# Kernel tuning notes

Hardware: AMD Instinct MI355X
Metric: run time of the kernel (lower is better)

Reference implementation:

```python
import jax, jax.numpy as jnp
import numpy as np

D_MODEL = 1024
NUM_HEADS = 16
D_HEAD = D_MODEL // NUM_HEADS
NEG_INF = float(np.finfo(np.float32).min)


def setup_inputs() -> dict:
    key = jax.random.key(0)
    ks = jax.random.split(key, 6)
    B, S = 2, 2048
    q = jax.random.normal(ks[0], (B, S, D_MODEL), dtype=jnp.float32)
    k = jax.random.normal(ks[1], (B, S, D_MODEL), dtype=jnp.float32)
    v = jax.random.normal(ks[2], (B, S, D_MODEL), dtype=jnp.float32)
    # causal boolean mask: True = attend
    attn_mask = jnp.tril(jnp.ones((S, S), dtype=bool))
    # nn.Linear(d_model, d_model, bias=False) weights: [out, in]; y = x @ W.T
    init_scale = 1.0 / np.sqrt(D_MODEL)
    Wq = jax.random.uniform(ks[3], (D_MODEL, D_MODEL), jnp.float32, -init_scale, init_scale)
    Wk = jax.random.uniform(ks[4], (D_MODEL, D_MODEL), jnp.float32, -init_scale, init_scale)
    Wv = jax.random.uniform(ks[5], (D_MODEL, D_MODEL), jnp.float32, -init_scale, init_scale)
    return {"query": q, "key": k, "value": v, "Wq": Wq, "Wk": Wk, "Wv": Wv,
            "attn_mask": attn_mask}


def _split_heads(x):
    # [B, S, D_MODEL] -> [B, H, S, d_head]
    B, S, _ = x.shape
    return x.reshape(B, S, NUM_HEADS, D_HEAD).transpose(0, 2, 1, 3)


def reference(query, key, value, Wq, Wk, Wv, attn_mask):
    B, Sq, _ = query.shape
    Sk = key.shape[1]
    q = _split_heads(query @ Wq.T)   # [B, H, Sq, dh]
    k = _split_heads(key @ Wk.T)     # [B, H, Sk, dh]
    v = _split_heads(value @ Wv.T)   # [B, H, Sk, dh]
    scale = 1.0 / np.sqrt(D_HEAD)
    scores = jnp.einsum('bhqd,bhkd->bhqk', q, k) * scale  # [B, H, Sq, Sk]
    scores = jnp.where(attn_mask[None, None, :, :], scores, NEG_INF)
    attn_weights = jax.nn.softmax(scores, axis=-1)
    ctx = jnp.einsum('bhqk,bhkd->bhqd', attn_weights, v)   # [B, H, Sq, dh]
    context = ctx.transpose(0, 2, 1, 3).reshape(B, Sq, D_MODEL)
    return context, attn_weights
```

## Files before the change

### kernel.cpp

```cpp
#include <hip/hip_runtime.h>
#include <hip/hip_bf16.h>

#define B_ 2
#define H_ 16
#define S_ 2048
#define DH_ 64
#define DM_ 1024
#define BH_ (B_*H_)
#define CTX_ELEMS (B_*S_*DM_)
#define ATTNW_ELEMS ((size_t)BH_*S_*S_)
#define HEAD_ELEMS (S_*DH_)

typedef __attribute__((ext_vector_type(4))) float  f32x4;
typedef __attribute__((ext_vector_type(8))) short  short8;
typedef __attribute__((ext_vector_type(4))) unsigned short ush4;
typedef unsigned short u16;
typedef unsigned int u32;

__device__ __forceinline__ u16 f2bf(float f) {
  union { __hip_bfloat16 h; u16 u; } cv;
  cv.h = __float2bfloat16(f);
  return cv.u;
}
__device__ __forceinline__ float bf2f(u16 u) {
  union { unsigned int i; float f; } cv;
  cv.i = ((unsigned int)u) << 16;
  return cv.f;
}

__device__ __forceinline__ void gload_lds16(const u16* g, u16* l) {
  __builtin_amdgcn_global_load_lds(
      (const __attribute__((address_space(1))) u32*)g,
      (__attribute__((address_space(3))) u32*)l, 16, 0, 0);
}

__global__ __launch_bounds__(256) void convert_all(
    const float* __restrict__ q, const float* __restrict__ k, const float* __restrict__ v,
    const float* __restrict__ wq, const float* __restrict__ wk, const float* __restrict__ wv,
    u16* __restrict__ xb, u16* __restrict__ wb)
{
  const int t = blockIdx.y;
  const float* s; u16* d; int nblk;
  if (t < 3) {
    s = (t == 0) ? wq : (t == 1) ? wk : wv;
    d = wb + (size_t)t * (DM_ * DM_);
    nblk = 512;
  } else {
    s = (t == 3) ? q : (t == 4) ? k : v;
    d = xb + (size_t)(t - 3) * ((size_t)B_ * S_ * DM_);
    nblk = 2048;
  }
  if (blockIdx.x >= nblk) return;
  const int i = (blockIdx.x * 256 + threadIdx.x) * 8;
  f32x4 a = *(const f32x4*)(s + i);
  f32x4 b = *(const f32x4*)(s + i + 4);
  short8 p;
#pragma unroll
  for (int j = 0; j < 4; ++j) { p[j] = (short)f2bf(a[j]); p[4 + j] = (short)f2bf(b[j]); }
  *(short8*)(d + i) = p;
}

__global__ __launch_bounds__(256) void proj_gemm(
    const u16* __restrict__ Xb, const u16* __restrict__ Wb,
    u16* __restrict__ O0, u16* __restrict__ O1, u16* __restrict__ O2)
{
  u16* O = (blockIdx.z == 0) ? O0 : (blockIdx.z == 1) ? O1 : O2;
  const u16* A = Xb + (size_t)blockIdx.z * ((size_t)B_ * S_ * DM_);
  const u16* W = Wb + (size_t)blockIdx.z * (DM_ * DM_);

  const int m0 = blockIdx.x * 128;
  const int n0 = blockIdx.y * 128;

  __shared__ u16 As[128 * 32];
  __shared__ u16 Bs[128 * 32];

  const int tid  = threadIdx.x;
  const int lane = tid & 63;
  const int w    = tid >> 6;
  const int wr   = w >> 1, wc = w & 1;
  const int l15  = lane & 15, l4 = lane >> 4;

  f32x4 acc[4][4];
#pragma unroll
  for (int i = 0; i < 4; ++i)
#pragma unroll
    for (int j = 0; j < 4; ++j) acc[i][j] = (f32x4){0.f, 0.f, 0.f, 0.f};

  const int srow = lane >> 2;
  const int scol = (lane & 3) * 8;
  const int ca = w * 2;
  const u16* ga0 = A + (size_t)(m0 + ca * 16 + srow) * DM_ + scol;
  const u16* ga1 = A + (size_t)(m0 + ca * 16 + 16 + srow) * DM_ + scol;
  const u16* gb0 = W + (size_t)(n0 + ca * 16 + srow) * DM_ + scol;
  const u16* gb1 = W + (size_t)(n0 + ca * 16 + 16 + srow) * DM_ + scol;

  for (int kb = 0; kb < DM_ / 32; ++kb) {
    const int k0 = kb * 32;
    gload_lds16(ga0 + k0, &As[ca * 512]);
    gload_lds16(ga1 + k0, &As[ca * 512 + 512]);
    gload_lds16(gb0 + k0, &Bs[ca * 512]);
    gload_lds16(gb1 + k0, &Bs[ca * 512 + 512]);
    __syncthreads();
    short8 af[4], bfr[4];
#pragma unroll
    for (int i = 0; i < 4; ++i)
      af[i] = *(const short8*)&As[(wr * 64 + i * 16 + l15) * 32 + l4 * 8];
#pragma unroll
    for (int j = 0; j < 4; ++j)
      bfr[j] = *(const short8*)&Bs[(wc * 64 + j * 16 + l15) * 32 + l4 * 8];
#pragma unroll
    for (int i = 0; i < 4; ++i)
#pragma unroll
      for (int j = 0; j < 4; ++j)
        acc[i][j] = __builtin_amdgcn_mfma_f32_16x16x32_bf16(af[i], bfr[j], acc[i][j], 0, 0, 0);
    __syncthreads();
  }

#pragma unroll
  for (int i = 0; i < 4; ++i) {
#pragma unroll
    for (int j = 0; j < 4; ++j) {
#pragma unroll
      for (int r = 0; r < 4; ++r) {
        const int grow = m0 + wr * 64 + i * 16 + l4 * 4 + r;
        const int gcol = n0 + wc * 64 + j * 16 + l15;
        const int b = grow >> 11, s = grow & (S_ - 1);
        const int h = gcol >> 6,  d = gcol & (DH_ - 1);
        O[(size_t)((b << 4) + h) * HEAD_ELEMS + (size_t)s * DH_ + d] = f2bf(acc[i][j][r]);
      }
    }
  }
}

__global__ __launch_bounds__(256) void transpose_v(const u16* __restrict__ vb,
                                                   u16* __restrict__ vt)
{
  __shared__ u16 T[64][72];
  const int bh = blockIdx.y;
  const int s0 = blockIdx.x * 64;
  const int tid = threadIdx.x;
  {
    const int sl = tid >> 2, dof = (tid & 3) * 16;
    const u16* src = vb + (size_t)bh * HEAD_ELEMS + (size_t)(s0 + sl) * DH_ + dof;
    *(short8*)&T[sl][dof]     = *(const short8*)(src);
    *(short8*)&T[sl][dof + 8] = *(const short8*)(src + 8);
  }
  __syncthreads();
  {
    const int dd = tid >> 2, sof = (tid & 3) * 16;
    u16* dst = vt + (size_t)bh * HEAD_ELEMS + (size_t)dd * S_ + s0 + sof;
    short8 t0, t1;
#pragma unroll
    for (int j = 0; j < 8; ++j) t0[j] = (short)T[sof + j][dd];
#pragma unroll
    for (int j = 0; j < 8; ++j) t1[j] = (short)T[sof + 8 + j][dd];
    *(short8*)(dst)     = t0;
    *(short8*)(dst + 8) = t1;
  }
}

#define PROW 2048
#define ATT_SMEM (16 * PROW * 2 + 16 * 4 + 64 * 4)

__global__ __launch_bounds__(256) void attn_kernel(
    const u16* __restrict__ qb, const u16* __restrict__ kb, const u16* __restrict__ vt,
    float* __restrict__ ctx, float* __restrict__ attnw)
{
  extern __shared__ u16 smem[];
  u16* P = smem;
  float* rinv    = (float*)(smem + 16 * PROW);
  float* partial = rinv + 16;

  const int lin = blockIdx.y * 128 + blockIdx.x;
  const int nl  = (lin & 7) * 512 + (lin >> 3);
  const int bh  = nl >> 7;
  const int qtl = nl & 127;
  const int qt  = 127 - qtl;

  const int tid = threadIdx.x;
  const int lane = tid & 63;
  const int w = tid >> 6;
  const int l15 = lane & 15, l4 = lane >> 4;

  const int NCC = ((qt * 16 + 16) + 127) >> 7;
  const int ncols = NCC << 7;
  const int qtmax = qt * 16 + 15;

  const u16* Qb = qb + (size_t)bh * HEAD_ELEMS + (size_t)(qt * 16) * DH_;
  const u16* Kb = kb + (size_t)bh * HEAD_ELEMS;
  const u16* Vt = vt + (size_t)bh * HEAD_ELEMS;

  const int qm = qtl;
  const int mcols = (((qm * 16 + 16) + 127) >> 7) << 7;
  float* zbase = attnw + (size_t)bh * ((size_t)S_ * S_) + (size_t)(qm * 16 + w * 4) * S_;
  const int zro = lane >> 5;
  const int zcl = (lane & 31) * 4;
  const f32x4 zv = (f32x4){0.f, 0.f, 0.f, 0.f};

  {
    short8 aQ0 = *(const short8*)(Qb + (size_t)l15 * DH_ + l4 * 8);
    short8 aQ1 = *(const short8*)(Qb + (size_t)l15 * DH_ + l4 * 8 + 32);
    const int qrow = l4 * 4;
    const int qabs = qt * 16 + qrow;
    float psum[4] = {0.f, 0.f, 0.f, 0.f};
    for (int ci = 0; ci < NCC; ++ci) {
      const int zc = mcols + (ci << 7);
      if (zc < S_) {
        __builtin_nontemporal_store(zv, (f32x4*)(zbase + (size_t)zro * S_ + zc + zcl));
        __builtin_nontemporal_store(zv, (f32x4*)(zbase + (size_t)(2 + zro) * S_ + zc + zcl));
      }
      const int col0 = (ci << 7) + w * 32;
#pragma unroll
      for (int t = 0; t < 2; ++t) {
        const int ct = col0 + t * 16;
        const int cg = ct + l15;
        if (ct <= qtmax) {
          const u16* kp = Kb + (size_t)cg * DH_ + l4 * 8;
          short8 b0 = *(const short8*)(kp);
          short8 b1 = *(const short8*)(kp + 32);
          f32x4 a0 = (f32x4){0.f, 0.f, 0.f, 0.f};
          f32x4 a1 = (f32x4){0.f, 0.f, 0.f, 0.f};
          a0 = __builtin_amdgcn_mfma_f32_16x16x32_bf16(aQ0, b0, a0, 0, 0, 0);
          a1 = __builtin_amdgcn_mfma_f32_16x16x32_bf16(aQ1, b1, a1, 0, 0, 0);
          const f32x4 a = a0 + a1;
#pragma unroll
          for (int r = 0; r < 4; ++r) {
            const float e = (cg <= qabs + r) ? __expf(a[r] * 0.125f) : 0.f;
            psum[r] += e;
            const int row = qrow + r;
            P[(row << 11) + (cg ^ ((row & 7) << 3))] = f2bf(e);
          }
        } else {
#pragma unroll
          for (int r = 0; r < 4; ++r) {
            const int row = qrow + r;
            P[(row << 11) + (cg ^ ((row & 7) << 3))] = 0;
          }
        }
      }
    }
#pragma unroll
    for (int r = 0; r < 4; ++r) {
      float s = psum[r];
      s += __shfl_xor(s, 1);
      s += __shfl_xor(s, 2);
      s += __shfl_xor(s, 4);
      s += __shfl_xor(s, 8);
      if (l15 == 0) partial[w * 16 + qrow + r] = s;
    }
  }
  __syncthreads();
  if (tid < 16) {
    const float l = partial[tid] + partial[16 + tid] + partial[32 + tid] + partial[48 + tid];
    rinv[tid] = 1.0f / l;
  }
  __syncthreads();

  if (w < 2) {
    for (int rr = 0; rr < 8; ++rr) {
      const int row = w * 8 + rr;
      const float inv = rinv[row];
      const int swz = (row & 7) << 3;
      const u16* prow = P + (row << 11);
      float* orow = attnw + (size_t)bh * ((size_t)S_ * S_) + (size_t)(qt * 16 + row) * S_;
      for (int c = 0; c < ncols; c += 256) {
        const int col = c + lane * 4;
        ush4 pv = *(const ush4*)(prow + (col ^ swz));
        const bool live = col < ncols;
        f32x4 o;
        o[0] = live ? bf2f(pv[0]) * inv : 0.f;
        o[1] = live ? bf2f(pv[1]) * inv : 0.f;
        o[2] = live ? bf2f(pv[2]) * inv : 0.f;
        o[3] = live ? bf2f(pv[3]) * inv : 0.f;
        if (live) __builtin_nontemporal_store(o, (f32x4*)(orow + col));
      }
    }
  } else {
    const int dq0 = (w - 2) * 2;
    f32x4 a00 = (f32x4){0.f, 0.f, 0.f, 0.f};
    f32x4 a01 = (f32x4){0.f, 0.f, 0.f, 0.f};
    f32x4 a10 = (f32x4){0.f, 0.f, 0.f, 0.f};
    f32x4 a11 = (f32x4){0.f, 0.f, 0.f, 0.f};
    const u16* vp0 = Vt + (size_t)(dq0 * 16 + l15) * S_ + l4 * 8;
    const u16* vp1 = vp0 + (size_t)16 * S_;
    const u16* prow = P + (l15 << 11);
    const int swz = (l15 & 7) << 3;
    for (int c = 0; c < ncols; c += 64) {
      short8 ap0 = *(const short8*)(prow + ((c + l4 * 8) ^ swz));
      short8 ap1 = *(const short8*)(prow + ((c + 32 + l4 * 8) ^ swz));
      short8 b00 = *(const short8*)(vp0 + c);
      short8 b01 = *(const short8*)(vp0 + c + 32);
      short8 b10 = *(const short8*)(vp1 + c);
      short8 b11 = *(const short8*)(vp1 + c + 32);
      a00 = __builtin_amdgcn_mfma_f32_16x16x32_bf16(ap0, b00, a00, 0, 0, 0);
      a10 = __builtin_amdgcn_mfma_f32_16x16x32_bf16(ap0, b10, a10, 0, 0, 0);
      a01 = __builtin_amdgcn_mfma_f32_16x16x32_bf16(ap1, b01, a01, 0, 0, 0);
      a11 = __builtin_amdgcn_mfma_f32_16x16x32_bf16(ap1, b11, a11, 0, 0, 0);
    }
    const f32x4 acc0 = a00 + a01;
    const f32x4 acc1 = a10 + a11;
    const int b = bh >> 4, h = bh & 15;
#pragma unroll
    for (int r = 0; r < 4; ++r) {
      const int rg = qt * 16 + l4 * 4 + r;
      const float inv = rinv[l4 * 4 + r];
      ctx[(size_t)(b * S_ + rg) * DM_ + h * 64 + dq0 * 16 + l15]        = acc0[r] * inv;
      ctx[(size_t)(b * S_ + rg) * DM_ + h * 64 + (dq0 + 1) * 16 + l15]  = acc1[r] * inv;
    }
  }
}

extern "C" void kernel_launch(void* const* d_in, const int* in_sizes, int n_in,
                              void* d_out, int out_size, void* d_ws, size_t ws_size,
                              hipStream_t stream) {
  const float* q  = (const float*)d_in[0];
  const float* k  = (const float*)d_in[1];
  const float* v  = (const float*)d_in[2];
  const float* Wq = (const float*)d_in[3];
  const float* Wk = (const float*)d_in[4];
  const float* Wv = (const float*)d_in[5];

  float* ctx   = (float*)d_out;
  float* attnw = ctx + CTX_ELEMS;

  u16* wb = (u16*)d_ws;
  u16* qb = wb + (size_t)3 * DM_ * DM_;
  u16* kb = qb + (size_t)BH_ * HEAD_ELEMS;
  u16* vb = kb + (size_t)BH_ * HEAD_ELEMS;
  u16* vt = vb + (size_t)BH_ * HEAD_ELEMS;
  u16* xb = (u16*)attnw;

  hipFuncSetAttribute(reinterpret_cast<const void*>(attn_kernel),
                      hipFuncAttributeMaxDynamicSharedMemorySize, ATT_SMEM);

  convert_all<<<dim3(2048, 6), 256, 0, stream>>>(q, k, v, Wq, Wk, Wv, xb, wb);
  proj_gemm<<<dim3(32, 8, 3), 256, 0, stream>>>(xb, wb, qb, kb, vb);
  transpose_v<<<dim3(32, 32), 256, 0, stream>>>(vb, vt);
  attn_kernel<<<dim3(128, 32), 256, ATT_SMEM, stream>>>(qb, kb, vt, ctx, attnw);
}
```

Before: 208.4 us.

## Make attention persistent with producer/consumer warps and double-buffered P tiles

Replaces the 4096 one-tile blocks with 256 persistent 512-thread blocks. Each block walks 16 query tiles of one head, strided so causal work is balanced. Four warps compute scores and exponentials into one of two LDS P buffers while the other four warps normalize and write attention weights, zero-fill the masked region, and do the PV MFMA for the previous tile. The goal is to overlap the QK/softmax phase with the store-heavy and PV phases and to cut launch and tail cost. The cost is 128 KB of LDS per block, so each CU holds far fewer blocks, and every tile step ends in a block-wide barrier.

```diff
diff --git a/kernel.cpp b/kernel.cpp
--- a/kernel.cpp
+++ b/kernel.cpp
@@ -159,153 +159,164 @@
   }
 }
 
-#define PROW 2048
-#define ATT_SMEM (16 * PROW * 2 + 16 * 4 + 64 * 4)
-
-__global__ __launch_bounds__(256) void attn_kernel(
+#define NTILES 16
+#define PBUF (16 * 2048)
+#define ATT_SMEM (2 * PBUF * 2 + 2 * 64 * 4)
+
+__global__ __launch_bounds__(512) void attn_kernel(
     const u16* __restrict__ qb, const u16* __restrict__ kb, const u16* __restrict__ vt,
     float* __restrict__ ctx, float* __restrict__ attnw)
 {
   extern __shared__ u16 smem[];
-  u16* P = smem;
-  float* rinv    = (float*)(smem + 16 * PROW);
-  float* partial = rinv + 16;
-
-  const int lin = blockIdx.y * 128 + blockIdx.x;
-  const int nl  = (lin & 7) * 512 + (lin >> 3);
-  const int bh  = nl >> 7;
-  const int qtl = nl & 127;
-  const int qt  = 127 - qtl;
+  u16* Pb = smem;
+  float* partial = (float*)(smem + 2 * PBUF);
+
+  const int lin = blockIdx.x;
+  const int nl  = (lin & 7) * 32 + (lin >> 3);
+  const int bh  = nl >> 3;
+  const int g   = nl & 7;
 
   const int tid = threadIdx.x;
   const int lane = tid & 63;
   const int w = tid >> 6;
   const int l15 = lane & 15, l4 = lane >> 4;
 
-  const int NCC = ((qt * 16 + 16) + 127) >> 7;
-  const int ncols = NCC << 7;
-  const int qtmax = qt * 16 + 15;
-
-  const u16* Qb = qb + (size_t)bh * HEAD_ELEMS + (size_t)(qt * 16) * DH_;
   const u16* Kb = kb + (size_t)bh * HEAD_ELEMS;
   const u16* Vt = vt + (size_t)bh * HEAD_ELEMS;
-
-  const int qm = qtl;
-  const int mcols = (((qm * 16 + 16) + 127) >> 7) << 7;
-  float* zbase = attnw + (size_t)bh * ((size_t)S_ * S_) + (size_t)(qm * 16 + w * 4) * S_;
-  const int zro = lane >> 5;
-  const int zcl = (lane & 31) * 4;
-  const f32x4 zv = (f32x4){0.f, 0.f, 0.f, 0.f};
-
-  {
-    short8 aQ0 = *(const short8*)(Qb + (size_t)l15 * DH_ + l4 * 8);
-    short8 aQ1 = *(const short8*)(Qb + (size_t)l15 * DH_ + l4 * 8 + 32);
-    const int qrow = l4 * 4;
-    const int qabs = qt * 16 + qrow;
-    float psum[4] = {0.f, 0.f, 0.f, 0.f};
-    for (int ci = 0; ci < NCC; ++ci) {
-      const int zc = mcols + (ci << 7);
-      if (zc < S_) {
-        __builtin_nontemporal_store(zv, (f32x4*)(zbase + (size_t)zro * S_ + zc + zcl));
-        __builtin_nontemporal_store(zv, (f32x4*)(zbase + (size_t)(2 + zro) * S_ + zc + zcl));
+  float* attnw_bh = attnw + (size_t)bh * ((size_t)S_ * S_);
+  const int bb = bh >> 4, hh = bh & 15;
+
+  for (int j = 0; j <= NTILES; ++j) {
+    __syncthreads();
+
+    if (w < 4) {
+      if (j < NTILES) {
+        const int qt = g + 8 * j;
+        const int NCC = j + 1;
+        const int qtmax = qt * 16 + 15;
+        const int buf = j & 1;
+        u16* P = Pb + buf * PBUF;
+        const u16* Qb = qb + (size_t)bh * HEAD_ELEMS + (size_t)(qt * 16) * DH_;
+
+        short8 aQ0 = *(const short8*)(Qb + (size_t)l15 * DH_ + l4 * 8);
+        short8 aQ1 = *(const short8*)(Qb + (size_t)l15 * DH_ + l4 * 8 + 32);
+        const int qrow = l4 * 4;
+        const int qabs = qt * 16 + qrow;
+        float psum[4] = {0.f, 0.f, 0.f, 0.f};
+        for (int ci = 0; ci < NCC; ++ci) {
+          const int col0 = (ci << 7) + w * 32;
+#pragma unroll
+          for (int t = 0; t < 2; ++t) {
+            const int ct = col0 + t * 16;
+            const int cg = ct + l15;
+            if (ct <= qtmax) {
+              const u16* kp = Kb + (size_t)cg * DH_ + l4 * 8;
+              short8 b0 = *(const short8*)(kp);
+              short8 b1 = *(const short8*)(kp + 32);
+              f32x4 a0 = (f32x4){0.f, 0.f, 0.f, 0.f};
+              f32x4 a1 = (f32x4){0.f, 0.f, 0.f, 0.f};
+              a0 = __builtin_amdgcn_mfma_f32_16x16x32_bf16(aQ0, b0, a0, 0, 0, 0);
+              a1 = __builtin_amdgcn_mfma_f32_16x16x32_bf16(aQ1, b1, a1, 0, 0, 0);
+              const f32x4 a = a0 + a1;
+#pragma unroll
+              for (int r = 0; r < 4; ++r) {
+                const float e = (cg <= qabs + r) ? __expf(a[r] * 0.125f) : 0.f;
+                psum[r] += e;
+                const int row = qrow + r;
+                P[(row << 11) + (cg ^ ((row & 7) << 3))] = f2bf(e);
+              }
+            } else {
+#pragma unroll
+              for (int r = 0; r < 4; ++r) {
+                const int row = qrow + r;
+                P[(row << 11) + (cg ^ ((row & 7) << 3))] = 0;
+              }
+            }
+          }
+        }
+#pragma unroll
+        for (int r = 0; r < 4; ++r) {
+          float s = psum[r];
+          s += __shfl_xor(s, 1);
+          s += __shfl_xor(s, 2);
+          s += __shfl_xor(s, 4);
+          s += __shfl_xor(s, 8);
+          if (l15 == 0) partial[buf * 64 + w * 16 + qrow + r] = s;
+        }
       }
-      const int col0 = (ci << 7) + w * 32;
-#pragma unroll
-      for (int t = 0; t < 2; ++t) {
-        const int ct = col0 + t * 16;
-        const int cg = ct + l15;
-        if (ct <= qtmax) {
-          const u16* kp = Kb + (size_t)cg * DH_ + l4 * 8;
-          short8 b0 = *(const short8*)(kp);
-          short8 b1 = *(const short8*)(kp + 32);
-          f32x4 a0 = (f32x4){0.f, 0.f, 0.f, 0.f};
-          f32x4 a1 = (f32x4){0.f, 0.f, 0.f, 0.f};
-          a0 = __builtin_amdgcn_mfma_f32_16x16x32_bf16(aQ0, b0, a0, 0, 0, 0);
-          a1 = __builtin_amdgcn_mfma_f32_16x16x32_bf16(aQ1, b1, a1, 0, 0, 0);
-          const f32x4 a = a0 + a1;
-#pragma unroll
-          for (int r = 0; r < 4; ++r) {
-            const float e = (cg <= qabs + r) ? __expf(a[r] * 0.125f) : 0.f;
-            psum[r] += e;
-            const int row = qrow + r;
-            P[(row << 11) + (cg ^ ((row & 7) << 3))] = f2bf(e);
+    } else if (j > 0) {
+      const int qt = g + 8 * (j - 1);
+      const int ncols = 128 * j;
+      const int buf = (j - 1) & 1;
+      const u16* P = Pb + buf * PBUF;
+      const float* pa = partial + buf * 64;
+
+      if (w < 6) {
+        const int cw = w - 4;
+        for (int rr = 0; rr < 8; ++rr) {
+          const int row = cw * 8 + rr;
+          const float inv = 1.0f / (pa[row] + pa[16 + row] + pa[32 + row] + pa[48 + row]);
+          const int swz = (row & 7) << 3;
+          const u16* prow = P + (row << 11);
+          float* orow = attnw_bh + (size_t)(qt * 16 + row) * S_;
+          for (int c = 0; c < ncols; c += 256) {
+            const int col = c + lane * 4;
+            ush4 pv = *(const ush4*)(prow + (col ^ swz));
+            const bool live = col < ncols;
+            f32x4 o;
+            o[0] = live ? bf2f(pv[0]) * inv : 0.f;
+            o[1] = live ? bf2f(pv[1]) * inv : 0.f;
+            o[2] = live ? bf2f(pv[2]) * inv : 0.f;
+            o[3] = live ? bf2f(pv[3]) * inv : 0.f;
+            if (live) __builtin_nontemporal_store(o, (f32x4*)(orow + col));
           }
-        } else {
-#pragma unroll
-          for (int r = 0; r < 4; ++r) {
-            const int row = qrow + r;
-            P[(row << 11) + (cg ^ ((row & 7) << 3))] = 0;
-          }
+        }
+        const int qm = 127 - qt;
+        const int mcols = S_ - ncols + 128;
+        const f32x4 zv = (f32x4){0.f, 0.f, 0.f, 0.f};
+        for (int rr = 0; rr < 8; ++rr) {
+          float* zrow = attnw_bh + (size_t)(qm * 16 + cw * 8 + rr) * S_;
+          for (int c = mcols + lane * 4; c < S_; c += 256)
+            __builtin_nontemporal_store(zv, (f32x4*)(zrow + c));
+        }
+      } else {
+        const int dq0 = (w - 6) * 2;
+        float invr[4];
+#pragma unroll
+        for (int r = 0; r < 4; ++r) {
+          const int row = l4 * 4 + r;
+          invr[r] = 1.0f / (pa[row] + pa[16 + row] + pa[32 + row] + pa[48 + row]);
+        }
+        f32x4 a00 = (f32x4){0.f, 0.f, 0.f, 0.f};
+        f32x4 a01 = (f32x4){0.f, 0.f, 0.f, 0.f};
+        f32x4 a10 = (f32x4){0.f, 0.f, 0.f, 0.f};
+        f32x4 a11 = (f32x4){0.f, 0.f, 0.f, 0.f};
+        const u16* vp0 = Vt + (size_t)(dq0 * 16 + l15) * S_ + l4 * 8;
+        const u16* vp1 = vp0 + (size_t)16 * S_;
+        const u16* prow = P + (l15 << 11);
+        const int swz = (l15 & 7) << 3;
+        for (int c = 0; c < ncols; c += 64) {
+          short8 ap0 = *(const short8*)(prow + ((c + l4 * 8) ^ swz));
+          short8 ap1 = *(const short8*)(prow + ((c + 32 + l4 * 8) ^ swz));
+          short8 b00 = *(const short8*)(vp0 + c);
+          short8 b01 = *(const short8*)(vp0 + c + 32);
+          short8 b10 = *(const short8*)(vp1 + c);
+          short8 b11 = *(const short8*)(vp1 + c + 32);
+          a00 = __builtin_amdgcn_mfma_f32_16x16x32_bf16(ap0, b00, a00, 0, 0, 0);
+          a10 = __builtin_amdgcn_mfma_f32_16x16x32_bf16(ap0, b10, a10, 0, 0, 0);
+          a01 = __builtin_amdgcn_mfma_f32_16x16x32_bf16(ap1, b01, a01, 0, 0, 0);
+          a11 = __builtin_amdgcn_mfma_f32_16x16x32_bf16(ap1, b11, a11, 0, 0, 0);
+        }
+        const f32x4 acc0 = a00 + a01;
+        const f32x4 acc1 = a10 + a11;
+#pragma unroll
+        for (int r = 0; r < 4; ++r) {
+          const int rg = qt * 16 + l4 * 4 + r;
+          float* cbase = ctx + (size_t)(bb * S_ + rg) * DM_ + hh * 64;
+          cbase[dq0 * 16 + l15]       = acc0[r] * invr[r];
+          cbase[(dq0 + 1) * 16 + l15] = acc1[r] * invr[r];
         }
       }
-    }
-#pragma unroll
-    for (int r = 0; r < 4; ++r) {
-      float s = psum[r];
-      s += __shfl_xor(s, 1);
-      s += __shfl_xor(s, 2);
-      s += __shfl_xor(s, 4);
-      s += __shfl_xor(s, 8);
-      if (l15 == 0) partial[w * 16 + qrow + r] = s;
-    }
-  }
-  __syncthreads();
-  if (tid < 16) {
-    const float l = partial[tid] + partial[16 + tid] + partial[32 + tid] + partial[48 + tid];
-    rinv[tid] = 1.0f / l;
-  }
-  __syncthreads();
-
-  if (w < 2) {
-    for (int rr = 0; rr < 8; ++rr) {
-      const int row = w * 8 + rr;
-      const float inv = rinv[row];
-      const int swz = (row & 7) << 3;
-      const u16* prow = P + (row << 11);
-      float* orow = attnw + (size_t)bh * ((size_t)S_ * S_) + (size_t)(qt * 16 + row) * S_;
-      for (int c = 0; c < ncols; c += 256) {
-        const int col = c + lane * 4;
-        ush4 pv = *(const ush4*)(prow + (col ^ swz));
-        const bool live = col < ncols;
-        f32x4 o;
-        o[0] = live ? bf2f(pv[0]) * inv : 0.f;
-        o[1] = live ? bf2f(pv[1]) * inv : 0.f;
-        o[2] = live ? bf2f(pv[2]) * inv : 0.f;
-        o[3] = live ? bf2f(pv[3]) * inv : 0.f;
-        if (live) __builtin_nontemporal_store(o, (f32x4*)(orow + col));
-      }
-    }
-  } else {
-    const int dq0 = (w - 2) * 2;
-    f32x4 a00 = (f32x4){0.f, 0.f, 0.f, 0.f};
-    f32x4 a01 = (f32x4){0.f, 0.f, 0.f, 0.f};
-    f32x4 a10 = (f32x4){0.f, 0.f, 0.f, 0.f};
-    f32x4 a11 = (f32x4){0.f, 0.f, 0.f, 0.f};
-    const u16* vp0 = Vt + (size_t)(dq0 * 16 + l15) * S_ + l4 * 8;
-    const u16* vp1 = vp0 + (size_t)16 * S_;
-    const u16* prow = P + (l15 << 11);
-    const int swz = (l15 & 7) << 3;
-    for (int c = 0; c < ncols; c += 64) {
-      short8 ap0 = *(const short8*)(prow + ((c + l4 * 8) ^ swz));
-      short8 ap1 = *(const short8*)(prow + ((c + 32 + l4 * 8) ^ swz));
-      short8 b00 = *(const short8*)(vp0 + c);
-      short8 b01 = *(const short8*)(vp0 + c + 32);
-      short8 b10 = *(const short8*)(vp1 + c);
-      short8 b11 = *(const short8*)(vp1 + c + 32);
-      a00 = __builtin_amdgcn_mfma_f32_16x16x32_bf16(ap0, b00, a00, 0, 0, 0);
-      a10 = __builtin_amdgcn_mfma_f32_16x16x32_bf16(ap0, b10, a10, 0, 0, 0);
-      a01 = __builtin_amdgcn_mfma_f32_16x16x32_bf16(ap1, b01, a01, 0, 0, 0);
-      a11 = __builtin_amdgcn_mfma_f32_16x16x32_bf16(ap1, b11, a11, 0, 0, 0);
-    }
-    const f32x4 acc0 = a00 + a01;
-    const f32x4 acc1 = a10 + a11;
-    const int b = bh >> 4, h = bh & 15;
-#pragma unroll
-    for (int r = 0; r < 4; ++r) {
-      const int rg = qt * 16 + l4 * 4 + r;
-      const float inv = rinv[l4 * 4 + r];
-      ctx[(size_t)(b * S_ + rg) * DM_ + h * 64 + dq0 * 16 + l15]        = acc0[r] * inv;
-      ctx[(size_t)(b * S_ + rg) * DM_ + h * 64 + (dq0 + 1) * 16 + l15]  = acc1[r] * inv;
     }
   }
 }
@@ -336,5 +347,5 @@
   convert_all<<<dim3(2048, 6), 256, 0, stream>>>(q, k, v, Wq, Wk, Wv, xb, wb);
   proj_gemm<<<dim3(32, 8, 3), 256, 0, stream>>>(xb, wb, qb, kb, vb);
   transpose_v<<<dim3(32, 32), 256, 0, stream>>>(vb, vt);
-  attn_kernel<<<dim3(128, 32), 256, ATT_SMEM, stream>>>(qb, kb, vt, ctx, attnw);
-}
+  attn_kernel<<<256, 512, ATT_SMEM, stream>>>(qb, kb, vt, ctx, attnw);
+}
```

Measured after the change: 219.5 us. +5.3%, slower.
